# Performance work log

Hardware: AMD Instinct MI355X
Metric: run time of the kernel (lower is better)

## Reference

```python
import jax, jax.numpy as jnp
import numpy as np
from jax import lax

B, S, E = 8, 2048, 1024
NH, K = 4, 4
DH = E // NH  # 256


def setup_inputs() -> dict:
    key = jax.random.key(0)
    ks = jax.random.split(key, 8)
    sc = 0.02  # small_init-style scale
    return {
        "x": jax.random.normal(ks[0], (B, S, E), jnp.float32),
        "conv_w": jax.random.normal(ks[1], (K, 1, E), jnp.float32) * sc,  # depthwise (W,1,E)
        "conv_b": jnp.zeros((E,), jnp.float32),
        "fgate_w": jax.random.normal(ks[2], (NH, DH, DH), jnp.float32) * sc,
        "igate_w": jax.random.normal(ks[3], (NH, DH, DH), jnp.float32) * sc,
        "zgate_w": jax.random.normal(ks[4], (NH, DH, DH), jnp.float32) * sc,
        "ogate_w": jax.random.normal(ks[5], (NH, DH, DH), jnp.float32) * sc,
        "rkernel": jax.random.normal(ks[6], (NH, DH, 4 * DH), jnp.float32) * sc,
        "rbias": jnp.zeros((NH, 4, DH), jnp.float32),
        "gn_weight": jnp.ones((E,), jnp.float32),
    }


def _headwise(x, w):
    # LinearHeadwiseExpand, bias=False: einsum('...hd,hod->...ho')
    Bx, Sx, _ = x.shape
    return jnp.einsum('bshd,hod->bsho', x.reshape(Bx, Sx, NH, DH), w)


def reference(x, conv_w, conv_b, fgate_w, igate_w, zgate_w, ogate_w, rkernel, rbias, gn_weight):
    # --- causal depthwise conv1d + SiLU ---
    xp = jnp.pad(x, ((0, 0), (K - 1, 0), (0, 0)))  # left pad -> causal
    xc = lax.conv_general_dilated(
        xp, conv_w, window_strides=(1,), padding='VALID',
        dimension_numbers=('NWC', 'WIO', 'NWC'), feature_group_count=E) + conv_b
    x_conv = xc * jax.nn.sigmoid(xc)  # SiLU

    # --- headwise gate pre-activations (matches torch cat order [i,f,z,o]) ---
    gi = _headwise(x_conv, fgate_w)
    gf = _headwise(x_conv, igate_w)
    gz = _headwise(x, zgate_w)
    go = _headwise(x, ogate_w)
    gx = jnp.stack([gi, gf, gz, go], axis=3)      # (B,S,NH,4,DH)
    gx_t = jnp.moveaxis(gx, 1, 0)                 # (S,B,NH,4,DH)

    # --- stabilized exponential-gated sLSTM recurrence (xLSTM vanilla cell) ---
    z0 = jnp.zeros((B, NH, DH), x.dtype)

    def step(carry, xt):
        y, c, n, m = carry  # each (B,NH,DH)
        ry = jnp.einsum('bhd,hdk->bhk', y, rkernel).reshape(B, NH, 4, DH)
        raw = xt + ry + rbias
        ir, fr, zr, orr = raw[:, :, 0], raw[:, :, 1], raw[:, :, 2], raw[:, :, 3]
        logfplusm = m + jax.nn.log_sigmoid(fr)
        mnew = jnp.maximum(ir, logfplusm)
        ig = jnp.exp(ir - mnew)
        fg = jnp.exp(logfplusm - mnew)
        cnew = fg * c + ig * jnp.tanh(zr)
        nnew = fg * n + ig
        ynew = jax.nn.sigmoid(orr) * cnew / nnew
        return (ynew, cnew, nnew, mnew), ynew

    _, ys = lax.scan(step, (z0, z0, z0, z0), gx_t)  # ys: (S,B,NH,DH)
    y = jnp.moveaxis(ys, 0, 1)                       # (B,S,NH,DH)

    # --- MultiHeadLayerNorm: group_norm with num_groups=NH, weight only (no bias) ---
    mu = jnp.mean(y, axis=-1, keepdims=True)
    var = jnp.var(y, axis=-1, keepdims=True)
    yn = (y - mu) * lax.rsqrt(var + 1e-5)
    out = (yn * gn_weight.reshape(NH, DH)).reshape(B, S, E)
    return out
```

## Files before the change

### kernel.cpp

```cpp
#include <hip/hip_runtime.h>
#include <hip/hip_fp16.h>

#define BB 8
#define SS 2048
#define EE 1024
#define NHH 4
#define DHH 256

typedef _Float16 f16x2 __attribute__((ext_vector_type(2)));
typedef _Float16 f16x8 __attribute__((ext_vector_type(8)));
typedef float f32x4 __attribute__((ext_vector_type(4)));

__device__ __forceinline__ __half2 u2h2(unsigned int u) {
  union { unsigned int u; __half2 h; } c; c.u = u; return c.h;
}
__device__ __forceinline__ unsigned int h2u(__half2 h) {
  union { unsigned int u; __half2 h; } c; c.h = h; return c.u;
}
__device__ __forceinline__ f16x2 u2f(unsigned int u) {
  union { unsigned int u; f16x2 f; } c; c.u = u; return c.f;
}
__device__ __forceinline__ unsigned int pack2(float a, float b) {
  f16x2 f; f.x = (_Float16)a; f.y = (_Float16)b;
  union { f16x2 f; unsigned int u; } c; c.f = f; return c.u;
}
__device__ __forceinline__ float fdot2u(unsigned int w, unsigned int y, float acc) {
#if __has_builtin(__builtin_amdgcn_fdot2)
  return __builtin_amdgcn_fdot2(u2f(w), u2f(y), acc, false);
#else
  __half2 a = u2h2(w), b = u2h2(y);
  return acc + __low2float(a) * __low2float(b) + __high2float(a) * __high2float(b);
#endif
}

__global__ __launch_bounds__(256) void gates_gemm2(
    const float* __restrict__ x, const float* __restrict__ conv_w,
    const float* __restrict__ conv_b,
    const float* __restrict__ fgw, const float* __restrict__ igw,
    const float* __restrict__ zgw, const float* __restrict__ ogw,
    __half* __restrict__ gx)
{
  __shared__ float Xs[8][11][33];
  __shared__ __half As[2][64][40];
  __shared__ __half Bs[2][128][40];

  const int tid = threadIdx.x;
  const int mt  = blockIdx.x;
  const int nt2 = blockIdx.y;
  const int h   = blockIdx.z;
  const int s0  = mt << 3;
  const int n0  = nt2 << 7;

  const float* W0 = (n0 < 256) ? fgw : igw;
  const float* W1 = (n0 < 256) ? zgw : ogw;
  const int oobase = n0 & 255;

  const int w = tid >> 6, l = tid & 63;
  const int lrow = l & 15, kq = l >> 4;
  const int koff = kq << 3;

  f32x4 acc[2][2][4] = {};

  for (int d0 = 0; d0 < DHH; d0 += 32) {
    const int ebase = h * DHH + d0;

    for (int i = tid; i < 8 * 11 * 32; i += 256) {
      int kk = i & 31, rest = i >> 5;
      int b = rest / 11, si = rest - b * 11;
      int sg = s0 - 3 + si;
      float v = 0.f;
      if (sg >= 0) v = x[((size_t)b * SS + sg) * EE + ebase + kk];
      Xs[b][si][kk] = v;
    }
    for (int i = tid; i < 2 * 128 * 32; i += 256) {
      int p = i >> 12;
      int rem = i & 4095;
      int col = rem >> 5, k = rem & 31;
      const float* Wp = p ? W1 : W0;
      int oo = oobase + col;
      Bs[p][col][k] = __float2half(Wp[((size_t)h * DHH + oo) * DHH + d0 + k]);
    }
    __syncthreads();

    for (int i = tid; i < 2 * 64 * 32; i += 256) {
      int p = i >> 11;
      int rem = i & 2047;
      int kk = rem & 31, r = rem >> 5;
      int sl = r >> 3, b = r & 7;
      if (p == 0) {
        int e = ebase + kk;
        float xc = conv_b[e];
        xc = fmaf(Xs[b][sl + 0][kk], conv_w[0 * EE + e], xc);
        xc = fmaf(Xs[b][sl + 1][kk], conv_w[1 * EE + e], xc);
        xc = fmaf(Xs[b][sl + 2][kk], conv_w[2 * EE + e], xc);
        xc = fmaf(Xs[b][sl + 3][kk], conv_w[3 * EE + e], xc);
        float sg = 1.f / (1.f + __expf(-xc));
        As[0][r][kk] = __float2half(xc * sg);
      } else {
        As[1][r][kk] = __float2half(Xs[b][sl + 3][kk]);
      }
    }
    __syncthreads();

#pragma unroll
    for (int p = 0; p < 2; ++p) {
#pragma unroll
      for (int ct = 0; ct < 2; ++ct) {
        f16x8 bfrag = *(const f16x8*)&Bs[p][w * 32 + ct * 16 + lrow][koff];
#pragma unroll
        for (int mtl = 0; mtl < 4; ++mtl) {
          f16x8 afrag = *(const f16x8*)&As[p][mtl * 16 + lrow][koff];
          acc[p][ct][mtl] =
              __builtin_amdgcn_mfma_f32_16x16x32_f16(afrag, bfrag, acc[p][ct][mtl], 0, 0, 0);
        }
      }
    }
    __syncthreads();
  }

#pragma unroll
  for (int p = 0; p < 2; ++p) {
#pragma unroll
    for (int ct = 0; ct < 2; ++ct) {
#pragma unroll
      for (int mtl = 0; mtl < 4; ++mtl) {
#pragma unroll
        for (int j = 0; j < 4; ++j) {
          int row_loc = mtl * 16 + kq * 4 + j;
          int grow = mt * 64 + row_loc;
          int colg = n0 + w * 32 + ct * 16 + lrow;
          gx[(size_t)grow * 4096 + h * 1024 + p * 512 + colg] =
              __float2half(acc[p][ct][mtl][j]);
        }
      }
    }
  }
}

__global__
__attribute__((amdgpu_flat_work_group_size(512, 512), amdgpu_waves_per_eu(1)))
void slstm_scan(
    const float* __restrict__ rk,
    const float* __restrict__ rb,
    const __half* __restrict__ gx,
    float* __restrict__ out)
{
  extern __shared__ unsigned char smem[];
  uint4* wl4   = (uint4*)smem;
  __half* ypub = (__half*)(smem + 131072);

  const int t = threadIdx.x;
  const int b = blockIdx.x >> 2, h = blockIdx.x & 3;
  const int d = t >> 1, par = t & 1;
  const int kbase = par << 7;
  const float* Rh = rk + (size_t)h * DHH * 1024;

  unsigned int wv[3][64];
#pragma unroll
  for (int g = 0; g < 3; ++g) {
    const int col = g * 256 + d;
#pragma unroll
    for (int pp = 0; pp < 64; ++pp) {
      int k = kbase + 2 * pp;
      wv[g][pp] = pack2(Rh[(size_t)k * 1024 + col], Rh[(size_t)(k + 1) * 1024 + col]);
    }
  }
  {
    const int col = 3 * 256 + d;
    for (int q = 0; q < 16; ++q) {
      uint4 u;
      int k = kbase + 8 * q;
      u.x = pack2(Rh[(size_t)(k + 0) * 1024 + col], Rh[(size_t)(k + 1) * 1024 + col]);
      u.y = pack2(Rh[(size_t)(k + 2) * 1024 + col], Rh[(size_t)(k + 3) * 1024 + col]);
      u.z = pack2(Rh[(size_t)(k + 4) * 1024 + col], Rh[(size_t)(k + 5) * 1024 + col]);
      u.w = pack2(Rh[(size_t)(k + 6) * 1024 + col], Rh[(size_t)(k + 7) * 1024 + col]);
      wl4[q * 512 + t] = u;
    }
  }

  float rbv[4];
#pragma unroll
  for (int g = 0; g < 4; ++g) rbv[g] = rb[h * 1024 + g * 256 + d];

  float c = 0.f, n = 0.f, m = 0.f;
  if (t < 256) { ypub[t] = __float2half(0.f); ypub[256 + t] = __float2half(0.f); }
  __syncthreads();

  int cur = 0;
  const __half* pg = gx + ((size_t)b * NHH + h) * 1024;
  float cx[4];
#pragma unroll
  for (int g = 0; g < 4; ++g) cx[g] = __half2float(pg[g * 256 + d]);
  const size_t out_base = ((size_t)b * SS) * EE + h * DHH + d;

  for (int st = 0; st < SS; ++st) {
    const __half* pn = pg + ((st + 1 < SS) ? (size_t)(BB * NHH * 1024) : 0);
    __half nx[4];
#pragma unroll
    for (int g = 0; g < 4; ++g) nx[g] = pn[g * 256 + d];

    const uint4* yv = (const uint4*)(ypub + cur * 256) + (par << 4);
    float aA0 = 0.f, aB0 = 0.f, aA1 = 0.f, aB1 = 0.f;
    float aA2 = 0.f, aB2 = 0.f, aA3 = 0.f, aB3 = 0.f;
#pragma unroll
    for (int j = 0; j < 16; ++j) {
      uint4 yq = yv[j];
      uint4 wq = wl4[j * 512 + t];
      aA0 = fdot2u(wv[0][4 * j + 0], yq.x, aA0);
      aA1 = fdot2u(wv[1][4 * j + 0], yq.x, aA1);
      aA2 = fdot2u(wv[2][4 * j + 0], yq.x, aA2);
      aA3 = fdot2u(wq.x,             yq.x, aA3);
      aB0 = fdot2u(wv[0][4 * j + 1], yq.y, aB0);
      aB1 = fdot2u(wv[1][4 * j + 1], yq.y, aB1);
      aB2 = fdot2u(wv[2][4 * j + 1], yq.y, aB2);
      aB3 = fdot2u(wq.y,             yq.y, aB3);
      aA0 = fdot2u(wv[0][4 * j + 2], yq.z, aA0);
      aA1 = fdot2u(wv[1][4 * j + 2], yq.z, aA1);
      aA2 = fdot2u(wv[2][4 * j + 2], yq.z, aA2);
      aA3 = fdot2u(wq.z,             yq.z, aA3);
      aB0 = fdot2u(wv[0][4 * j + 3], yq.w, aB0);
      aB1 = fdot2u(wv[1][4 * j + 3], yq.w, aB1);
      aB2 = fdot2u(wv[2][4 * j + 3], yq.w, aB2);
      aB3 = fdot2u(wq.w,             yq.w, aB3);
    }

    float part0 = aA0 + aB0, part1 = aA1 + aB1;
    float part2 = aA2 + aB2, part3 = aA3 + aB3;
    float raw0 = part0 + __shfl_xor(part0, 1) + cx[0] + rbv[0];
    float raw1 = part1 + __shfl_xor(part1, 1) + cx[1] + rbv[1];
    float raw2 = part2 + __shfl_xor(part2, 1) + cx[2] + rbv[2];
    float raw3 = part3 + __shfl_xor(part3, 1) + cx[3] + rbv[3];

    float iv = raw0, fv = raw1, zv = raw2, ov = raw3;
    float ea = __expf(-fabsf(fv));
    float ls = fminf(fv, 0.f) - __logf(1.f + ea);
    float lfm = m + ls;
    float mn = fmaxf(iv, lfm);
    float ig = __expf(iv - mn);
    float fg = __expf(lfm - mn);
    float pz = __expf(-2.f * fabsf(zv));
    float tmag = __fdividef(1.f - pz, 1.f + pz);
    float th = (zv < 0.f) ? -tmag : tmag;
    c = fg * c + ig * th;
    n = fg * n + ig;
    float og = __fdividef(1.f, 1.f + __expf(-ov));
    float y = og * __fdividef(c, n);
    m = mn;

    if (par == 0) {
      out[out_base + (size_t)st * EE] = y;
      ypub[(cur ^ 1) * 256 + d] = __float2half(y);
    }
    __syncthreads();
    cur ^= 1;
    pg = pn;
#pragma unroll
    for (int g = 0; g < 4; ++g) cx[g] = __half2float(nx[g]);
  }
}

__global__ __launch_bounds__(256) void groupnorm(
    float* __restrict__ y, const float* __restrict__ gnw)
{
  const int row = blockIdx.x;
  const int t = threadIdx.x;
  float4 v = ((const float4*)y)[(size_t)row * 256 + t];
  float s = v.x + v.y + v.z + v.w;
  float q = v.x * v.x + v.y * v.y + v.z * v.z + v.w * v.w;
#pragma unroll
  for (int mask = 1; mask < 64; mask <<= 1) {
    s += __shfl_xor(s, mask, 64);
    q += __shfl_xor(q, mask, 64);
  }
  float mu = s * (1.f / 256.f);
  float var = q * (1.f / 256.f) - mu * mu;
  float rs = rsqrtf(var + 1e-5f);
  float4 g = ((const float4*)gnw)[t];
  float4 o;
  o.x = (v.x - mu) * rs * g.x;
  o.y = (v.y - mu) * rs * g.y;
  o.z = (v.z - mu) * rs * g.z;
  o.w = (v.w - mu) * rs * g.w;
  ((float4*)y)[(size_t)row * 256 + t] = o;
}

extern "C" void kernel_launch(void* const* d_in, const int* in_sizes, int n_in,
                              void* d_out, int out_size, void* d_ws, size_t ws_size,
                              hipStream_t stream) {
  const float* x      = (const float*)d_in[0];
  const float* conv_w = (const float*)d_in[1];
  const float* conv_b = (const float*)d_in[2];
  const float* fgw    = (const float*)d_in[3];
  const float* igw    = (const float*)d_in[4];
  const float* zgw    = (const float*)d_in[5];
  const float* ogw    = (const float*)d_in[6];
  const float* rk     = (const float*)d_in[7];
  const float* rb     = (const float*)d_in[8];
  const float* gnw    = (const float*)d_in[9];
  float* out = (float*)d_out;
  __half* gx = (__half*)d_ws;

  dim3 g1(256, 4, 4);
  gates_gemm2<<<g1, 256, 0, stream>>>(x, conv_w, conv_b, fgw, igw, zgw, ogw, gx);

  const int scan_lds = 131072 + 1024;
  (void)hipFuncSetAttribute(reinterpret_cast<const void*>(slstm_scan),
                            hipFuncAttributeMaxDynamicSharedMemorySize, scan_lds);
  slstm_scan<<<32, 512, scan_lds, stream>>>(rk, rb, gx, out);

  groupnorm<<<BB * SS, 256, 0, stream>>>(out, gnw);
}
```

Measured before the change: 3.947 ms.

## Move most recurrent weights from registers to pre-packed global/L2 reads in scan

Adds a pack_w kernel that converts the recurrent kernel into fp16 uint4 tiles in workspace. The scan now keeps only 48 register words for the i-gate, stores the f-gate in LDS, and reads the z/o gates and the rest of the i-gate from the packed global buffer on every step. This frees a large share of VGPRs that previously held 192 words of weights, at the cost of global/L2 loads inside the serial timestep loop. It also adds one extra small kernel launch.

```diff
diff --git a/kernel.cpp b/kernel.cpp
--- a/kernel.cpp
+++ b/kernel.cpp
@@ -31,6 +31,30 @@
   __half2 a = u2h2(w), b = u2h2(y);
   return acc + __low2float(a) * __low2float(b) + __high2float(a) * __high2float(b);
 #endif
+}
+
+__global__ __launch_bounds__(256) void pack_w(
+    const float* __restrict__ rk, uint4* __restrict__ wpk)
+{
+  int idx = blockIdx.x * 256 + threadIdx.x;
+  if (idx >= 4 * 36 * 512) return;
+  int t = idx & 511;
+  int c = (idx >> 9) % 36;
+  int h = idx / (36 * 512);
+  int d = t >> 1, par = t & 1, kbase = par << 7;
+  int g, j;
+  if (c < 4)       { g = 0; j = 12 + c; }
+  else if (c < 20) { g = 2; j = c - 4; }
+  else             { g = 3; j = c - 20; }
+  int k0 = kbase + j * 8;
+  int col = g * 256 + d;
+  const float* Rh = rk + (size_t)h * DHH * 1024;
+  uint4 u;
+  u.x = pack2(Rh[(size_t)(k0 + 0) * 1024 + col], Rh[(size_t)(k0 + 1) * 1024 + col]);
+  u.y = pack2(Rh[(size_t)(k0 + 2) * 1024 + col], Rh[(size_t)(k0 + 3) * 1024 + col]);
+  u.z = pack2(Rh[(size_t)(k0 + 4) * 1024 + col], Rh[(size_t)(k0 + 5) * 1024 + col]);
+  u.w = pack2(Rh[(size_t)(k0 + 6) * 1024 + col], Rh[(size_t)(k0 + 7) * 1024 + col]);
+  wpk[idx] = u;
 }
 
 __global__ __launch_bounds__(256) void gates_gemm2(
@@ -139,10 +163,11 @@
 
 __global__
 __attribute__((amdgpu_flat_work_group_size(512, 512), amdgpu_waves_per_eu(1)))
-void slstm_scan(
+void slstm_scan8(
     const float* __restrict__ rk,
     const float* __restrict__ rb,
     const __half* __restrict__ gx,
+    const uint4* __restrict__ wpk,
     float* __restrict__ out)
 {
   extern __shared__ unsigned char smem[];
@@ -154,19 +179,16 @@
   const int d = t >> 1, par = t & 1;
   const int kbase = par << 7;
   const float* Rh = rk + (size_t)h * DHH * 1024;
-
-  unsigned int wv[3][64];
-#pragma unroll
-  for (int g = 0; g < 3; ++g) {
-    const int col = g * 256 + d;
-#pragma unroll
-    for (int pp = 0; pp < 64; ++pp) {
-      int k = kbase + 2 * pp;
-      wv[g][pp] = pack2(Rh[(size_t)k * 1024 + col], Rh[(size_t)(k + 1) * 1024 + col]);
-    }
+  const uint4* wgh = wpk + (size_t)h * 36 * 512;
+
+  unsigned int wv[48];
+#pragma unroll
+  for (int pp = 0; pp < 48; ++pp) {
+    int k = kbase + 2 * pp;
+    wv[pp] = pack2(Rh[(size_t)k * 1024 + d], Rh[(size_t)(k + 1) * 1024 + d]);
   }
   {
-    const int col = 3 * 256 + d;
+    const int col = 256 + d;
     for (int q = 0; q < 16; ++q) {
       uint4 u;
       int k = kbase + 8 * q;
@@ -205,23 +227,33 @@
 #pragma unroll
     for (int j = 0; j < 16; ++j) {
       uint4 yq = yv[j];
-      uint4 wq = wl4[j * 512 + t];
-      aA0 = fdot2u(wv[0][4 * j + 0], yq.x, aA0);
-      aA1 = fdot2u(wv[1][4 * j + 0], yq.x, aA1);
-      aA2 = fdot2u(wv[2][4 * j + 0], yq.x, aA2);
-      aA3 = fdot2u(wq.x,             yq.x, aA3);
-      aB0 = fdot2u(wv[0][4 * j + 1], yq.y, aB0);
-      aB1 = fdot2u(wv[1][4 * j + 1], yq.y, aB1);
-      aB2 = fdot2u(wv[2][4 * j + 1], yq.y, aB2);
-      aB3 = fdot2u(wq.y,             yq.y, aB3);
-      aA0 = fdot2u(wv[0][4 * j + 2], yq.z, aA0);
-      aA1 = fdot2u(wv[1][4 * j + 2], yq.z, aA1);
-      aA2 = fdot2u(wv[2][4 * j + 2], yq.z, aA2);
-      aA3 = fdot2u(wq.z,             yq.z, aA3);
-      aB0 = fdot2u(wv[0][4 * j + 3], yq.w, aB0);
-      aB1 = fdot2u(wv[1][4 * j + 3], yq.w, aB1);
-      aB2 = fdot2u(wv[2][4 * j + 3], yq.w, aB2);
-      aB3 = fdot2u(wq.w,             yq.w, aB3);
+      uint4 wf = wl4[j * 512 + t];
+      uint4 wz = wgh[(4 + j) * 512 + t];
+      uint4 wo = wgh[(20 + j) * 512 + t];
+      if (j < 12) {
+        aA0 = fdot2u(wv[4 * j + 0], yq.x, aA0);
+        aB0 = fdot2u(wv[4 * j + 1], yq.y, aB0);
+        aA0 = fdot2u(wv[4 * j + 2], yq.z, aA0);
+        aB0 = fdot2u(wv[4 * j + 3], yq.w, aB0);
+      } else {
+        uint4 wi = wgh[(j - 12) * 512 + t];
+        aA0 = fdot2u(wi.x, yq.x, aA0);
+        aB0 = fdot2u(wi.y, yq.y, aB0);
+        aA0 = fdot2u(wi.z, yq.z, aA0);
+        aB0 = fdot2u(wi.w, yq.w, aB0);
+      }
+      aA1 = fdot2u(wf.x, yq.x, aA1);
+      aB1 = fdot2u(wf.y, yq.y, aB1);
+      aA1 = fdot2u(wf.z, yq.z, aA1);
+      aB1 = fdot2u(wf.w, yq.w, aB1);
+      aA2 = fdot2u(wz.x, yq.x, aA2);
+      aB2 = fdot2u(wz.y, yq.y, aB2);
+      aA2 = fdot2u(wz.z, yq.z, aA2);
+      aB2 = fdot2u(wz.w, yq.w, aB2);
+      aA3 = fdot2u(wo.x, yq.x, aA3);
+      aB3 = fdot2u(wo.y, yq.y, aB3);
+      aA3 = fdot2u(wo.z, yq.z, aA3);
+      aB3 = fdot2u(wo.w, yq.w, aB3);
     }
 
     float part0 = aA0 + aB0, part1 = aA1 + aB1;
@@ -299,14 +331,17 @@
   const float* gnw    = (const float*)d_in[9];
   float* out = (float*)d_out;
   __half* gx = (__half*)d_ws;
+  uint4* wpk = (uint4*)((char*)d_ws + 134217728);
+
+  pack_w<<<288, 256, 0, stream>>>(rk, wpk);
 
   dim3 g1(256, 4, 4);
   gates_gemm2<<<g1, 256, 0, stream>>>(x, conv_w, conv_b, fgw, igw, zgw, ogw, gx);
 
   const int scan_lds = 131072 + 1024;
-  (void)hipFuncSetAttribute(reinterpret_cast<const void*>(slstm_scan),
+  (void)hipFuncSetAttribute(reinterpret_cast<const void*>(slstm_scan8),
                             hipFuncAttributeMaxDynamicSharedMemorySize, scan_lds);
-  slstm_scan<<<32, 512, scan_lds, stream>>>(rk, rb, gx, out);
+  slstm_scan8<<<32, 512, scan_lds, stream>>>(rk, rb, gx, wpk, out);
 
   groupnorm<<<BB * SS, 256, 0, stream>>>(out, gnw);
 }
```

New measurement: 4.304 ms. 1.09x slower.

## Fuse gates GEMM, sLSTM scan and groupnorm into one persistent kernel with progress flags

Applied to the files above, without the earlier changes.

Merges the three kernels into a single launch. Blocks 0-31 run the recurrent scan, the next 2048 blocks compute the gate GEMM tiles, and the last 64 blocks do groupnorm. Global atomic counters record finished GEMM chunks of 256 timesteps and finished scan chunks, so the scan can start once its first chunk of gates is ready and groupnorm can overlap the tail of the scan. The aim is to hide the GEMM and groupnorm time behind the latency-bound serial scan. The cost is spin-waiting with bounded timeouts, and the design depends on the scan blocks being co-resident with the producers and dispatched first to avoid deadlock. Each block also reserves about 132KB of LDS, which limits how many GEMM blocks can be resident at once.

```diff
diff --git a/kernel.cpp b/kernel.cpp
--- a/kernel.cpp
+++ b/kernel.cpp
@@ -33,255 +33,315 @@
 #endif
 }
 
-__global__ __launch_bounds__(256) void gates_gemm2(
+__global__
+__attribute__((amdgpu_flat_work_group_size(512, 512), amdgpu_waves_per_eu(1)))
+void mega(
     const float* __restrict__ x, const float* __restrict__ conv_w,
     const float* __restrict__ conv_b,
     const float* __restrict__ fgw, const float* __restrict__ igw,
     const float* __restrict__ zgw, const float* __restrict__ ogw,
-    __half* __restrict__ gx)
+    const float* __restrict__ rk, const float* __restrict__ rb,
+    const float* __restrict__ gnw,
+    __half* __restrict__ gx, float* __restrict__ out,
+    unsigned int* __restrict__ prog, unsigned int* __restrict__ sprog)
 {
-  __shared__ float Xs[8][11][33];
-  __shared__ __half As[2][64][40];
-  __shared__ __half Bs[2][128][40];
-
+  extern __shared__ unsigned char sm[];
+  const int bid = blockIdx.x;
   const int tid = threadIdx.x;
-  const int mt  = blockIdx.x;
-  const int nt2 = blockIdx.y;
-  const int h   = blockIdx.z;
-  const int s0  = mt << 3;
-  const int n0  = nt2 << 7;
-
-  const float* W0 = (n0 < 256) ? fgw : igw;
-  const float* W1 = (n0 < 256) ? zgw : ogw;
-  const int oobase = n0 & 255;
-
-  const int w = tid >> 6, l = tid & 63;
-  const int lrow = l & 15, kq = l >> 4;
-  const int koff = kq << 3;
-
-  f32x4 acc[2][2][4] = {};
-
-  for (int d0 = 0; d0 < DHH; d0 += 32) {
-    const int ebase = h * DHH + d0;
-
-    for (int i = tid; i < 8 * 11 * 32; i += 256) {
-      int kk = i & 31, rest = i >> 5;
-      int b = rest / 11, si = rest - b * 11;
-      int sg = s0 - 3 + si;
-      float v = 0.f;
-      if (sg >= 0) v = x[((size_t)b * SS + sg) * EE + ebase + kk];
-      Xs[b][si][kk] = v;
-    }
-    for (int i = tid; i < 2 * 128 * 32; i += 256) {
-      int p = i >> 12;
-      int rem = i & 4095;
-      int col = rem >> 5, k = rem & 31;
-      const float* Wp = p ? W1 : W0;
-      int oo = oobase + col;
-      Bs[p][col][k] = __float2half(Wp[((size_t)h * DHH + oo) * DHH + d0 + k]);
-    }
+
+  if (bid >= 32 && bid < 32 + 2048) {
+    const int half = tid >> 8, ltid = tid & 255;
+    const int ti = (bid - 32) * 2 + half;
+    const int mtg = ti >> 4;
+    const int rest = ti & 15;
+    const int nt2 = rest >> 2, h = rest & 3;
+    const int s0 = mtg << 3;
+    const int n0 = nt2 << 7;
+
+    unsigned char* base = sm + half * 42368;
+    float* Xs = (float*)base;
+    __half* As = (__half*)(base + 11648);
+    __half* Bs = (__half*)(base + 11648 + 10240);
+
+    const float* W0 = (n0 < 256) ? fgw : igw;
+    const float* W1 = (n0 < 256) ? zgw : ogw;
+    const int oobase = n0 & 255;
+
+    const int lw = (tid >> 6) & 3, l = tid & 63;
+    const int lrow = l & 15, kq = l >> 4;
+    const int koff = kq << 3;
+
+    f32x4 acc[2][2][4] = {};
+
+    for (int d0 = 0; d0 < DHH; d0 += 32) {
+      const int ebase = h * DHH + d0;
+
+      for (int i = ltid; i < 8 * 11 * 32; i += 256) {
+        int kk = i & 31, rest2 = i >> 5;
+        int b = rest2 / 11, si = rest2 - b * 11;
+        int sg = s0 - 3 + si;
+        float v = 0.f;
+        if (sg >= 0) v = x[((size_t)b * SS + sg) * EE + ebase + kk];
+        Xs[(b * 11 + si) * 33 + kk] = v;
+      }
+      for (int i = ltid; i < 2 * 128 * 32; i += 256) {
+        int p = i >> 12;
+        int rem = i & 4095;
+        int col = rem >> 5, k = rem & 31;
+        const float* Wp = p ? W1 : W0;
+        int oo = oobase + col;
+        Bs[(p * 128 + col) * 40 + k] =
+            __float2half(Wp[((size_t)h * DHH + oo) * DHH + d0 + k]);
+      }
+      __syncthreads();
+
+      for (int i = ltid; i < 2 * 64 * 32; i += 256) {
+        int p = i >> 11;
+        int rem = i & 2047;
+        int kk = rem & 31, r = rem >> 5;
+        int sl = r >> 3, b = r & 7;
+        if (p == 0) {
+          int e = ebase + kk;
+          float xc = conv_b[e];
+          xc = fmaf(Xs[(b * 11 + sl + 0) * 33 + kk], conv_w[0 * EE + e], xc);
+          xc = fmaf(Xs[(b * 11 + sl + 1) * 33 + kk], conv_w[1 * EE + e], xc);
+          xc = fmaf(Xs[(b * 11 + sl + 2) * 33 + kk], conv_w[2 * EE + e], xc);
+          xc = fmaf(Xs[(b * 11 + sl + 3) * 33 + kk], conv_w[3 * EE + e], xc);
+          float sg = 1.f / (1.f + __expf(-xc));
+          As[(0 * 64 + r) * 40 + kk] = __float2half(xc * sg);
+        } else {
+          As[(1 * 64 + r) * 40 + kk] = __float2half(Xs[(b * 11 + sl + 3) * 33 + kk]);
+        }
+      }
+      __syncthreads();
+
+#pragma unroll
+      for (int p = 0; p < 2; ++p) {
+#pragma unroll
+        for (int ct = 0; ct < 2; ++ct) {
+          f16x8 bfrag = *(const f16x8*)&Bs[(p * 128 + lw * 32 + ct * 16 + lrow) * 40 + koff];
+#pragma unroll
+          for (int mtl = 0; mtl < 4; ++mtl) {
+            f16x8 afrag = *(const f16x8*)&As[(p * 64 + mtl * 16 + lrow) * 40 + koff];
+            acc[p][ct][mtl] =
+                __builtin_amdgcn_mfma_f32_16x16x32_f16(afrag, bfrag, acc[p][ct][mtl], 0, 0, 0);
+          }
+        }
+      }
+      __syncthreads();
+    }
+
+#pragma unroll
+    for (int p = 0; p < 2; ++p) {
+#pragma unroll
+      for (int ct = 0; ct < 2; ++ct) {
+#pragma unroll
+        for (int mtl = 0; mtl < 4; ++mtl) {
+#pragma unroll
+          for (int j = 0; j < 4; ++j) {
+            int row_loc = mtl * 16 + kq * 4 + j;
+            int grow = mtg * 64 + row_loc;
+            int colg = n0 + lw * 32 + ct * 16 + lrow;
+            gx[(size_t)grow * 4096 + h * 1024 + p * 512 + colg] =
+                __float2half(acc[p][ct][mtl][j]);
+          }
+        }
+      }
+    }
+
     __syncthreads();
-
-    for (int i = tid; i < 2 * 64 * 32; i += 256) {
-      int p = i >> 11;
-      int rem = i & 2047;
-      int kk = rem & 31, r = rem >> 5;
-      int sl = r >> 3, b = r & 7;
-      if (p == 0) {
-        int e = ebase + kk;
-        float xc = conv_b[e];
-        xc = fmaf(Xs[b][sl + 0][kk], conv_w[0 * EE + e], xc);
-        xc = fmaf(Xs[b][sl + 1][kk], conv_w[1 * EE + e], xc);
-        xc = fmaf(Xs[b][sl + 2][kk], conv_w[2 * EE + e], xc);
-        xc = fmaf(Xs[b][sl + 3][kk], conv_w[3 * EE + e], xc);
-        float sg = 1.f / (1.f + __expf(-xc));
-        As[0][r][kk] = __float2half(xc * sg);
-      } else {
-        As[1][r][kk] = __float2half(Xs[b][sl + 3][kk]);
-      }
-    }
+    if (ltid == 0)
+      __hip_atomic_fetch_add(&prog[mtg >> 5], 1u,
+                             __ATOMIC_RELEASE, __HIP_MEMORY_SCOPE_AGENT);
+    return;
+  }
+
+  if (bid < 32) {
+    uint4* wl4   = (uint4*)sm;
+    __half* ypub = (__half*)(sm + 131072);
+
+    const int t = tid;
+    const int b = bid >> 2, h = bid & 3;
+    const int d = t >> 1, par = t & 1;
+    const int kbase = par << 7;
+    const float* Rh = rk + (size_t)h * DHH * 1024;
+
+    unsigned int wv[3][64];
+#pragma unroll
+    for (int g = 0; g < 3; ++g) {
+      const int col = g * 256 + d;
+#pragma unroll
+      for (int pp = 0; pp < 64; ++pp) {
+        int k = kbase + 2 * pp;
+        wv[g][pp] = pack2(Rh[(size_t)k * 1024 + col], Rh[(size_t)(k + 1) * 1024 + col]);
+      }
+    }
+    {
+      const int col = 3 * 256 + d;
+      for (int q = 0; q < 16; ++q) {
+        uint4 u;
+        int k = kbase + 8 * q;
+        u.x = pack2(Rh[(size_t)(k + 0) * 1024 + col], Rh[(size_t)(k + 1) * 1024 + col]);
+        u.y = pack2(Rh[(size_t)(k + 2) * 1024 + col], Rh[(size_t)(k + 3) * 1024 + col]);
+        u.z = pack2(Rh[(size_t)(k + 4) * 1024 + col], Rh[(size_t)(k + 5) * 1024 + col]);
+        u.w = pack2(Rh[(size_t)(k + 6) * 1024 + col], Rh[(size_t)(k + 7) * 1024 + col]);
+        wl4[q * 512 + t] = u;
+      }
+    }
+
+    float rbv[4];
+#pragma unroll
+    for (int g = 0; g < 4; ++g) rbv[g] = rb[h * 1024 + g * 256 + d];
+
+    float c = 0.f, n = 0.f, m = 0.f;
+    if (t < 256) { ypub[t] = __float2half(0.f); ypub[256 + t] = __float2half(0.f); }
     __syncthreads();
 
-#pragma unroll
-    for (int p = 0; p < 2; ++p) {
-#pragma unroll
-      for (int ct = 0; ct < 2; ++ct) {
-        f16x8 bfrag = *(const f16x8*)&Bs[p][w * 32 + ct * 16 + lrow][koff];
-#pragma unroll
-        for (int mtl = 0; mtl < 4; ++mtl) {
-          f16x8 afrag = *(const f16x8*)&As[p][mtl * 16 + lrow][koff];
-          acc[p][ct][mtl] =
-              __builtin_amdgcn_mfma_f32_16x16x32_f16(afrag, bfrag, acc[p][ct][mtl], 0, 0, 0);
+    if (t == 0) {
+      int it = 0;
+      while (__hip_atomic_load(&prog[0], __ATOMIC_ACQUIRE,
+                               __HIP_MEMORY_SCOPE_AGENT) < 512u) {
+        __builtin_amdgcn_s_sleep(8);
+        if (++it > (1 << 20)) break;
+      }
+    }
+    __syncthreads();
+    int curc = 0;
+
+    int cur = 0;
+    const __half* pg = gx + ((size_t)b * NHH + h) * 1024;
+    float cx[4];
+#pragma unroll
+    for (int g = 0; g < 4; ++g) cx[g] = __half2float(pg[g * 256 + d]);
+    const size_t out_base = ((size_t)b * SS) * EE + h * DHH + d;
+
+    for (int st = 0; st < SS; ++st) {
+      {
+        int needc = ((st + 1 < SS) ? st + 1 : SS - 1) >> 8;
+        if (needc != curc) {
+          if (t == 0) {
+            int it = 0;
+            while (__hip_atomic_load(&prog[needc], __ATOMIC_ACQUIRE,
+                                     __HIP_MEMORY_SCOPE_AGENT) < 512u) {
+              __builtin_amdgcn_s_sleep(8);
+              if (++it > (1 << 20)) break;
+            }
+          }
+          __syncthreads();
+          curc = needc;
         }
       }
+
+      const __half* pn = pg + ((st + 1 < SS) ? (size_t)(BB * NHH * 1024) : 0);
+      __half nx[4];
+#pragma unroll
+      for (int g = 0; g < 4; ++g) nx[g] = pn[g * 256 + d];
+
+      const uint4* yv = (const uint4*)(ypub + cur * 256) + (par << 4);
+      float aA0 = 0.f, aB0 = 0.f, aA1 = 0.f, aB1 = 0.f;
+      float aA2 = 0.f, aB2 = 0.f, aA3 = 0.f, aB3 = 0.f;
+#pragma unroll
+      for (int j = 0; j < 16; ++j) {
+        uint4 yq = yv[j];
+        uint4 wq = wl4[j * 512 + t];
+        aA0 = fdot2u(wv[0][4 * j + 0], yq.x, aA0);
+        aA1 = fdot2u(wv[1][4 * j + 0], yq.x, aA1);
+        aA2 = fdot2u(wv[2][4 * j + 0], yq.x, aA2);
+        aA3 = fdot2u(wq.x,             yq.x, aA3);
+        aB0 = fdot2u(wv[0][4 * j + 1], yq.y, aB0);
+        aB1 = fdot2u(wv[1][4 * j + 1], yq.y, aB1);
+        aB2 = fdot2u(wv[2][4 * j + 1], yq.y, aB2);
+        aB3 = fdot2u(wq.y,             yq.y, aB3);
+        aA0 = fdot2u(wv[0][4 * j + 2], yq.z, aA0);
+        aA1 = fdot2u(wv[1][4 * j + 2], yq.z, aA1);
+        aA2 = fdot2u(wv[2][4 * j + 2], yq.z, aA2);
+        aA3 = fdot2u(wq.z,             yq.z, aA3);
+        aB0 = fdot2u(wv[0][4 * j + 3], yq.w, aB0);
+        aB1 = fdot2u(wv[1][4 * j + 3], yq.w, aB1);
+        aB2 = fdot2u(wv[2][4 * j + 3], yq.w, aB2);
+        aB3 = fdot2u(wq.w,             yq.w, aB3);
+      }
+
+      float part0 = aA0 + aB0, part1 = aA1 + aB1;
+      float part2 = aA2 + aB2, part3 = aA3 + aB3;
+      float raw0 = part0 + __shfl_xor(part0, 1) + cx[0] + rbv[0];
+      float raw1 = part1 + __shfl_xor(part1, 1) + cx[1] + rbv[1];
+      float raw2 = part2 + __shfl_xor(part2, 1) + cx[2] + rbv[2];
+      float raw3 = part3 + __shfl_xor(part3, 1) + cx[3] + rbv[3];
+
+      float iv = raw0, fv = raw1, zv = raw2, ov = raw3;
+      float ea = __expf(-fabsf(fv));
+      float ls = fminf(fv, 0.f) - __logf(1.f + ea);
+      float lfm = m + ls;
+      float mn = fmaxf(iv, lfm);
+      float ig = __expf(iv - mn);
+      float fg = __expf(lfm - mn);
+      float pz = __expf(-2.f * fabsf(zv));
+      float tmag = __fdividef(1.f - pz, 1.f + pz);
+      float th = (zv < 0.f) ? -tmag : tmag;
+      c = fg * c + ig * th;
+      n = fg * n + ig;
+      float og = __fdividef(1.f, 1.f + __expf(-ov));
+      float y = og * __fdividef(c, n);
+      m = mn;
+
+      if (par == 0) {
+        out[out_base + (size_t)st * EE] = y;
+        ypub[(cur ^ 1) * 256 + d] = __float2half(y);
+      }
+      __syncthreads();
+
+      if ((st & 255) == 255 && t == 0) {
+        __hip_atomic_fetch_add(&sprog[(st >> 8) * 8 + b], 1u,
+                               __ATOMIC_RELEASE, __HIP_MEMORY_SCOPE_AGENT);
+      }
+
+      cur ^= 1;
+      pg = pn;
+#pragma unroll
+      for (int g = 0; g < 4; ++g) cx[g] = __half2float(nx[g]);
+    }
+    return;
+  }
+
+  {
+    const int g = bid - (32 + 2048);
+    const int cchunk = g >> 3, b = g & 7;
+    const int half = tid >> 8, tt = tid & 255;
+
+    if (tid == 0) {
+      int it = 0;
+      while (__hip_atomic_load(&sprog[cchunk * 8 + b], __ATOMIC_ACQUIRE,
+                               __HIP_MEMORY_SCOPE_AGENT) < 4u) {
+        __builtin_amdgcn_s_sleep(16);
+        if (++it > (1 << 20)) break;
+      }
     }
     __syncthreads();
+
+    for (int sr = 0; sr < 256; sr += 2) {
+      const int s = cchunk * 256 + sr + half;
+      const size_t row = (size_t)b * SS + s;
+      float4 v = ((const float4*)out)[row * 256 + tt];
+      float sacc = v.x + v.y + v.z + v.w;
+      float qacc = v.x * v.x + v.y * v.y + v.z * v.z + v.w * v.w;
+#pragma unroll
+      for (int mask = 1; mask < 64; mask <<= 1) {
+        sacc += __shfl_xor(sacc, mask, 64);
+        qacc += __shfl_xor(qacc, mask, 64);
+      }
+      float mu = sacc * (1.f / 256.f);
+      float var = qacc * (1.f / 256.f) - mu * mu;
+      float rs = rsqrtf(var + 1e-5f);
+      float4 gw = ((const float4*)gnw)[tt];
+      float4 o;
+      o.x = (v.x - mu) * rs * gw.x;
+      o.y = (v.y - mu) * rs * gw.y;
+      o.z = (v.z - mu) * rs * gw.z;
+      o.w = (v.w - mu) * rs * gw.w;
+      ((float4*)out)[row * 256 + tt] = o;
+    }
   }
-
-#pragma unroll
-  for (int p = 0; p < 2; ++p) {
-#pragma unroll
-    for (int ct = 0; ct < 2; ++ct) {
-#pragma unroll
-      for (int mtl = 0; mtl < 4; ++mtl) {
-#pragma unroll
-        for (int j = 0; j < 4; ++j) {
-          int row_loc = mtl * 16 + kq * 4 + j;
-          int grow = mt * 64 + row_loc;
-          int colg = n0 + w * 32 + ct * 16 + lrow;
-          gx[(size_t)grow * 4096 + h * 1024 + p * 512 + colg] =
-              __float2half(acc[p][ct][mtl][j]);
-        }
-      }
-    }
-  }
-}
-
-__global__
-__attribute__((amdgpu_flat_work_group_size(512, 512), amdgpu_waves_per_eu(1)))
-void slstm_scan(
-    const float* __restrict__ rk,
-    const float* __restrict__ rb,
-    const __half* __restrict__ gx,
-    float* __restrict__ out)
-{
-  extern __shared__ unsigned char smem[];
-  uint4* wl4   = (uint4*)smem;
-  __half* ypub = (__half*)(smem + 131072);
-
-  const int t = threadIdx.x;
-  const int b = blockIdx.x >> 2, h = blockIdx.x & 3;
-  const int d = t >> 1, par = t & 1;
-  const int kbase = par << 7;
-  const float* Rh = rk + (size_t)h * DHH * 1024;
-
-  unsigned int wv[3][64];
-#pragma unroll
-  for (int g = 0; g < 3; ++g) {
-    const int col = g * 256 + d;
-#pragma unroll
-    for (int pp = 0; pp < 64; ++pp) {
-      int k = kbase + 2 * pp;
-      wv[g][pp] = pack2(Rh[(size_t)k * 1024 + col], Rh[(size_t)(k + 1) * 1024 + col]);
-    }
-  }
-  {
-    const int col = 3 * 256 + d;
-    for (int q = 0; q < 16; ++q) {
-      uint4 u;
-      int k = kbase + 8 * q;
-      u.x = pack2(Rh[(size_t)(k + 0) * 1024 + col], Rh[(size_t)(k + 1) * 1024 + col]);
-      u.y = pack2(Rh[(size_t)(k + 2) * 1024 + col], Rh[(size_t)(k + 3) * 1024 + col]);
-      u.z = pack2(Rh[(size_t)(k + 4) * 1024 + col], Rh[(size_t)(k + 5) * 1024 + col]);
-      u.w = pack2(Rh[(size_t)(k + 6) * 1024 + col], Rh[(size_t)(k + 7) * 1024 + col]);
-      wl4[q * 512 + t] = u;
-    }
-  }
-
-  float rbv[4];
-#pragma unroll
-  for (int g = 0; g < 4; ++g) rbv[g] = rb[h * 1024 + g * 256 + d];
-
-  float c = 0.f, n = 0.f, m = 0.f;
-  if (t < 256) { ypub[t] = __float2half(0.f); ypub[256 + t] = __float2half(0.f); }
-  __syncthreads();
-
-  int cur = 0;
-  const __half* pg = gx + ((size_t)b * NHH + h) * 1024;
-  float cx[4];
-#pragma unroll
-  for (int g = 0; g < 4; ++g) cx[g] = __half2float(pg[g * 256 + d]);
-  const size_t out_base = ((size_t)b * SS) * EE + h * DHH + d;
-
-  for (int st = 0; st < SS; ++st) {
-    const __half* pn = pg + ((st + 1 < SS) ? (size_t)(BB * NHH * 1024) : 0);
-    __half nx[4];
-#pragma unroll
-    for (int g = 0; g < 4; ++g) nx[g] = pn[g * 256 + d];
-
-    const uint4* yv = (const uint4*)(ypub + cur * 256) + (par << 4);
-    float aA0 = 0.f, aB0 = 0.f, aA1 = 0.f, aB1 = 0.f;
-    float aA2 = 0.f, aB2 = 0.f, aA3 = 0.f, aB3 = 0.f;
-#pragma unroll
-    for (int j = 0; j < 16; ++j) {
-      uint4 yq = yv[j];
-      uint4 wq = wl4[j * 512 + t];
-      aA0 = fdot2u(wv[0][4 * j + 0], yq.x, aA0);
-      aA1 = fdot2u(wv[1][4 * j + 0], yq.x, aA1);
-      aA2 = fdot2u(wv[2][4 * j + 0], yq.x, aA2);
-      aA3 = fdot2u(wq.x,             yq.x, aA3);
-      aB0 = fdot2u(wv[0][4 * j + 1], yq.y, aB0);
-      aB1 = fdot2u(wv[1][4 * j + 1], yq.y, aB1);
-      aB2 = fdot2u(wv[2][4 * j + 1], yq.y, aB2);
-      aB3 = fdot2u(wq.y,             yq.y, aB3);
-      aA0 = fdot2u(wv[0][4 * j + 2], yq.z, aA0);
-      aA1 = fdot2u(wv[1][4 * j + 2], yq.z, aA1);
-      aA2 = fdot2u(wv[2][4 * j + 2], yq.z, aA2);
-      aA3 = fdot2u(wq.z,             yq.z, aA3);
-      aB0 = fdot2u(wv[0][4 * j + 3], yq.w, aB0);
-      aB1 = fdot2u(wv[1][4 * j + 3], yq.w, aB1);
-      aB2 = fdot2u(wv[2][4 * j + 3], yq.w, aB2);
-      aB3 = fdot2u(wq.w,             yq.w, aB3);
-    }
-
-    float part0 = aA0 + aB0, part1 = aA1 + aB1;
-    float part2 = aA2 + aB2, part3 = aA3 + aB3;
-    float raw0 = part0 + __shfl_xor(part0, 1) + cx[0] + rbv[0];
-    float raw1 = part1 + __shfl_xor(part1, 1) + cx[1] + rbv[1];
-    float raw2 = part2 + __shfl_xor(part2, 1) + cx[2] + rbv[2];
-    float raw3 = part3 + __shfl_xor(part3, 1) + cx[3] + rbv[3];
-
-    float iv = raw0, fv = raw1, zv = raw2, ov = raw3;
-    float ea = __expf(-fabsf(fv));
-    float ls = fminf(fv, 0.f) - __logf(1.f + ea);
-    float lfm = m + ls;
-    float mn = fmaxf(iv, lfm);
-    float ig = __expf(iv - mn);
-    float fg = __expf(lfm - mn);
-    float pz = __expf(-2.f * fabsf(zv));
-    float tmag = __fdividef(1.f - pz, 1.f + pz);
-    float th = (zv < 0.f) ? -tmag : tmag;
-    c = fg * c + ig * th;
-    n = fg * n + ig;
-    float og = __fdividef(1.f, 1.f + __expf(-ov));
-    float y = og * __fdividef(c, n);
-    m = mn;
-
-    if (par == 0) {
-      out[out_base + (size_t)st * EE] = y;
-      ypub[(cur ^ 1) * 256 + d] = __float2half(y);
-    }
-    __syncthreads();
-    cur ^= 1;
-    pg = pn;
-#pragma unroll
-    for (int g = 0; g < 4; ++g) cx[g] = __half2float(nx[g]);
-  }
-}
-
-__global__ __launch_bounds__(256) void groupnorm(
-    float* __restrict__ y, const float* __restrict__ gnw)
-{
-  const int row = blockIdx.x;
-  const int t = threadIdx.x;
-  float4 v = ((const float4*)y)[(size_t)row * 256 + t];
-  float s = v.x + v.y + v.z + v.w;
-  float q = v.x * v.x + v.y * v.y + v.z * v.z + v.w * v.w;
-#pragma unroll
-  for (int mask = 1; mask < 64; mask <<= 1) {
-    s += __shfl_xor(s, mask, 64);
-    q += __shfl_xor(q, mask, 64);
-  }
-  float mu = s * (1.f / 256.f);
-  float var = q * (1.f / 256.f) - mu * mu;
-  float rs = rsqrtf(var + 1e-5f);
-  float4 g = ((const float4*)gnw)[t];
-  float4 o;
-  o.x = (v.x - mu) * rs * g.x;
-  o.y = (v.y - mu) * rs * g.y;
-  o.z = (v.z - mu) * rs * g.z;
-  o.w = (v.w - mu) * rs * g.w;
-  ((float4*)y)[(size_t)row * 256 + t] = o;
 }
 
 extern "C" void kernel_launch(void* const* d_in, const int* in_sizes, int n_in,
@@ -298,15 +358,16 @@
   const float* rb     = (const float*)d_in[8];
   const float* gnw    = (const float*)d_in[9];
   float* out = (float*)d_out;
+
   __half* gx = (__half*)d_ws;
-
-  dim3 g1(256, 4, 4);
-  gates_gemm2<<<g1, 256, 0, stream>>>(x, conv_w, conv_b, fgw, igw, zgw, ogw, gx);
-
-  const int scan_lds = 131072 + 1024;
-  (void)hipFuncSetAttribute(reinterpret_cast<const void*>(slstm_scan),
-                            hipFuncAttributeMaxDynamicSharedMemorySize, scan_lds);
-  slstm_scan<<<32, 512, scan_lds, stream>>>(rk, rb, gx, out);
-
-  groupnorm<<<BB * SS, 256, 0, stream>>>(out, gnw);
-}
+  unsigned int* prog  = (unsigned int*)((char*)d_ws + 134217728);
+  unsigned int* sprog = (unsigned int*)((char*)d_ws + 134217728 + 128);
+
+  (void)hipMemsetAsync(prog, 0, 4096, stream);
+
+  const int lds = 132096;
+  (void)hipFuncSetAttribute(reinterpret_cast<const void*>(mega),
+                            hipFuncAttributeMaxDynamicSharedMemorySize, lds);
+  mega<<<32 + 2048 + 64, 512, lds, stream>>>(
+      x, conv_w, conv_b, fgw, igw, zgw, ogw, rk, rb, gnw, gx, out, prog, sprog);
+}
```

New measurement: 3.714 ms (median of 2 runs). 5.9% less time.
